# Kernel optimization log

Measured on AMD Instinct MI355X. Metric: run time of the kernel, lower is better.

The kernel has to match this reference:

```python
import jax, jax.numpy as jnp
import numpy as np

# static config (mirrors init_kwargs)
F_T, S = 8, 24            # video_shape = (F_T, S, S)
K, DIL = 3, 1             # kernel_size, dilation (same for all 3 axes)
HEADS, DHEAD, DIM = 8, 64, 512
INNER = HEADS * DHEAD
PAD = DIL * (K - 1)       # causal: pad 2 at the FRONT of each spatial axis
KJ = K ** 3               # 27 neighbors per query
N_VID = F_T * S * S       # 4608 video tokens


def causal_pad(t):
    # t: [B, D, F, S, S] -> pad front of f/h/w axes (torch F.pad (PAD*?,0) causal layout)
    return jnp.pad(t, ((0, 0), (0, 0), (PAD, 0), (PAD, 0), (PAD, 0)))


def unfold3d(t):
    # torch unfoldNd equivalent. t: [B, D, F+PAD, S+PAD, S+PAD]
    # returns [B, N_VID, KJ, D]; kernel offsets ordered (kf, kh, kw) w fastest,
    # matching torch unfold's channel-major / kernel-minor layout after the
    # rearrange 'b (d j) i -> b i j d'.
    sl = []
    for i in range(K):
        for j in range(K):
            for kk in range(K):
                sl.append(t[:, :, i * DIL:i * DIL + F_T,
                                  j * DIL:j * DIL + S,
                                  kk * DIL:kk * DIL + S])
    u = jnp.stack(sl, axis=2)                      # [B, D, KJ, F, S, S]
    B, D = t.shape[0], t.shape[1]
    u = u.reshape(B, D, KJ, N_VID)
    return jnp.transpose(u, (0, 3, 2, 1))          # [B, N_VID, KJ, D]


def make_mask():
    # True where the neighbor falls into zero padding (out-of-range / future under causal pad)
    ones = jnp.ones((1, 1, F_T, S, S), jnp.float32)
    u = unfold3d(causal_pad(ones))[0, :, :, 0]     # [N_VID, KJ]
    m = u == 0.0
    return jnp.pad(m, ((0, 0), (1, 0)), constant_values=False)  # bos col never masked


def stable_softmax(t, alpha=32.0 ** 2):
    t = t / alpha
    t = t - jax.lax.stop_gradient(jnp.max(t, axis=-1, keepdims=True))
    return jax.nn.softmax(t * alpha, axis=-1)


def setup_inputs() -> dict:
    key = jax.random.key(0)
    ks = jax.random.split(key, 9)
    return {
        "x": jax.random.normal(ks[0], (1, N_VID + 1, DIM), jnp.float32),
        "Wq": jax.random.normal(ks[1], (DIM, INNER), jnp.float32) * 0.02,
        "Wkv": jax.random.normal(ks[2], (DIM, 2 * INNER), jnp.float32) * 0.02,
        "W_th": jax.random.normal(ks[3], (HEADS, HEADS), jnp.float32) * 0.2,
        "Wout": jax.random.normal(ks[4], (INNER, DIM), jnp.float32) * 0.02,
        "bout": jax.random.normal(ks[5], (DIM,), jnp.float32) * 0.02,
        "ax1": jax.random.normal(ks[6], (K, HEADS), jnp.float32),
        "ax2": jax.random.normal(ks[7], (K, HEADS), jnp.float32),
        "ax3": jax.random.normal(ks[8], (K, HEADS), jnp.float32),
    }


def reference(x, Wq, Wkv, W_th, Wout, bout, ax1, ax2, ax3):
    b, n, _ = x.shape                       # b=1, n = 1 + N_VID (no extra padding)
    h, d = HEADS, DHEAD
    scale = d ** -0.5

    q = x @ Wq
    k, v = jnp.split(x @ Wkv, 2, axis=-1)

    def to_heads(t):  # 'b n (h d) -> (b h) n d'
        return t.reshape(b, n, h, d).transpose(0, 2, 1, 3).reshape(b * h, n, d)

    q, k, v = map(to_heads, (q, k, v))
    q = q[:, 1:] * scale                    # drop bos query
    k_bos, v_bos = k[:, :1], v[:, :1]       # [bh, 1, d]
    k, v = k[:, 1:], v[:, 1:]

    def to_vid(t):  # 'b (f h w) d -> b d f h w'
        return t.reshape(b * h, F_T, S, S, d).transpose(0, 4, 1, 2, 3)

    ku = unfold3d(causal_pad(to_vid(k)))    # [bh, N, KJ, d]
    vu = unfold3d(causal_pad(to_vid(v)))
    N = ku.shape[1]

    kb = jnp.broadcast_to(k_bos[:, :, None, :], (b * h, N, 1, d))
    vb = jnp.broadcast_to(v_bos[:, :, None, :], (b * h, N, 1, d))
    ku = jnp.concatenate([kb, ku], axis=2)  # [bh, N, KJ+1, d]
    vu = jnp.concatenate([vb, vu], axis=2)

    sim = jnp.einsum('bid,bijd->bij', q, ku)                 # [bh, N, KJ+1]

    # axial relative position bias over the 3x3x3 kernel, pad 0 for bos column
    rel = (ax1[:, None, None, :] + ax2[None, :, None, :] + ax3[None, None, :, :])
    rel = rel.reshape(KJ, h)                                 # [27, h]
    bias = jnp.pad(rel.T[:, None, :], ((0, 0), (0, 0), (1, 0)))  # [h, 1, KJ+1]

    sim = sim.reshape(b, h, N, KJ + 1) + bias[None]
    mask = make_mask()                                       # [N, KJ+1]
    sim = jnp.where(mask[None, None], -jnp.finfo(sim.dtype).max, sim)

    attn = stable_softmax(sim)                               # [b, h, N, KJ+1]
    attn = jnp.einsum('hg,bgij->bhij', W_th, attn)           # talking heads 1x1 conv

    out = jnp.einsum('bhij,bhijd->bhid', attn, vu.reshape(b, h, N, KJ + 1, d))
    out = jnp.concatenate([v_bos.reshape(b, h, 1, d), out], axis=2)  # re-attach bos value
    out = out.transpose(0, 2, 1, 3).reshape(b, n, h * d)     # '(b h) n d -> b n (h d)'
    return out @ Wout + bout
```

## Files before the change

kernel.cpp:

```cpp
#include <hip/hip_runtime.h>
#include <hip/hip_bf16.h>


constexpr int TFR   = 8;
constexpr int SDIM  = 24;
constexpr int NVID  = TFR * SDIM * SDIM;
constexpr int NTOK  = NVID + 1;
constexpr int NH    = 8;
constexpr int DM    = 512;
constexpr int NJ    = 28;

typedef __attribute__((ext_vector_type(8))) short bf16x8;
typedef __attribute__((ext_vector_type(8))) unsigned short ushort8;
typedef __attribute__((ext_vector_type(4))) float f32x4;

typedef const __attribute__((address_space(1))) unsigned int* gas_ptr;
typedef __attribute__((address_space(3))) unsigned int* las_ptr;

__device__ __forceinline__ float bf2f(unsigned short u) {
    return __uint_as_float((unsigned)u << 16);
}
__device__ __forceinline__ unsigned short f2bf(float f) {
    __hip_bfloat16 h = __float2bfloat16(f);
    return reinterpret_cast<unsigned short&>(h);
}

__global__ __launch_bounds__(256)
void prep_w(const float* __restrict__ Wq, const float* __restrict__ Wkv,
            const float* __restrict__ Wout,
            __hip_bfloat16* __restrict__ Wqkvt, __hip_bfloat16* __restrict__ Woutt)
{
    __shared__ float t[32][33];
    const int tid = threadIdx.x;
    int tb = blockIdx.x;
    const float* W; __hip_bfloat16* Wt; int Nd, tX, rowOff;
    if (tb < 256)      { W = Wq;   Wt = Wqkvt; Nd = 512;  tX = 16; rowOff = 0;   }
    else if (tb < 768) { tb -= 256; W = Wkv;  Wt = Wqkvt; Nd = 1024; tX = 32; rowOff = 512; }
    else               { tb -= 768; W = Wout; Wt = Woutt; Nd = 512;  tX = 16; rowOff = 0;   }
    const int n0 = (tb % tX) * 32, k0 = (tb / tX) * 32;
    const int r  = tid >> 3;
    const int c4 = (tid & 7) * 4;
    const float4 v = *(const float4*)(W + (size_t)(k0 + r) * Nd + n0 + c4);
    t[r][c4 + 0] = v.x; t[r][c4 + 1] = v.y; t[r][c4 + 2] = v.z; t[r][c4 + 3] = v.w;
    __syncthreads();
    #pragma unroll
    for (int j = 0; j < 4; ++j)
        Wt[(size_t)(rowOff + n0 + r) * 512 + k0 + c4 + j] = __float2bfloat16(t[c4 + j][r]);
}

__global__ __launch_bounds__(256)
void gemm_qkv(const float* __restrict__ A, const __hip_bfloat16* __restrict__ Bt,
              float* __restrict__ Cq, __hip_bfloat16* __restrict__ Ckv, int M)
{
    constexpr int BM = 128, BN = 128, BK = 64, PITCH = 72, K = 512;
    __shared__ short As[BM * PITCH];
    __shared__ __align__(16) short Bs[BN * BK];

    const int tid  = threadIdx.x;
    const int m0   = blockIdx.x * BM;
    const int n0   = blockIdx.y * BN;
    const int lane = tid & 63;
    const int wave = tid >> 6;
    const int wm   = (wave >> 1) * 64;
    const int wn   = (wave & 1) * 64;
    const int col  = lane & 15;
    const int quad = lane >> 4;

    f32x4 acc[4][4] = {};

    for (int k0 = 0; k0 < K; k0 += BK) {
        #pragma unroll
        for (int it = 0; it < 4; ++it) {
            const int idx = it * 256 + tid;
            const int r   = idx >> 3;
            const int u   = (idx & 7) ^ (r & 7);
            const __hip_bfloat16* gp = Bt + (size_t)(n0 + r) * K + k0 + u * 8;
            __builtin_amdgcn_global_load_lds(
                (gas_ptr)gp, (las_ptr)&Bs[(it * 256 + wave * 64) * 8], 16, 0, 0);
        }
        #pragma unroll
        for (int r = 0; r < 4; ++r) {
            const int m  = (tid >> 3) + r * 32;
            const int k8 = (tid & 7) * 8;
            const int gm = (m0 + m < M) ? (m0 + m) : (M - 1);
            const float4 f0 = *(const float4*)(A + (size_t)gm * K + k0 + k8);
            const float4 f1 = *(const float4*)(A + (size_t)gm * K + k0 + k8 + 4);
            unsigned short v[8] = { f2bf(f0.x), f2bf(f0.y), f2bf(f0.z), f2bf(f0.w),
                                    f2bf(f1.x), f2bf(f1.y), f2bf(f1.z), f2bf(f1.w) };
            *(ushort8*)(&As[m * PITCH + k8]) = *(const ushort8*)v;
        }
        __syncthreads();

        #pragma unroll
        for (int ks = 0; ks < 2; ++ks) {
            bf16x8 af[4], bfr[4];
            #pragma unroll
            for (int mt = 0; mt < 4; ++mt)
                af[mt] = *(const bf16x8*)(&As[(wm + mt * 16 + col) * PITCH + ks * 32 + quad * 8]);
            #pragma unroll
            for (int nt = 0; nt < 4; ++nt) {
                const int r = wn + nt * 16 + col;
                const int u = (ks * 4 + quad) ^ (r & 7);
                bfr[nt] = *(const bf16x8*)(&Bs[r * BK + u * 8]);
            }
            #pragma unroll
            for (int mt = 0; mt < 4; ++mt)
                #pragma unroll
                for (int nt = 0; nt < 4; ++nt)
                    acc[mt][nt] = __builtin_amdgcn_mfma_f32_16x16x32_bf16(
                        af[mt], bfr[nt], acc[mt][nt], 0, 0, 0);
        }
        __syncthreads();
    }

    const bool isQ = (n0 < 512);
    #pragma unroll
    for (int mt = 0; mt < 4; ++mt) {
        #pragma unroll
        for (int r = 0; r < 4; ++r) {
            const int row = m0 + wm + mt * 16 + quad * 4 + r;
            if (row >= M) continue;
            #pragma unroll
            for (int nt = 0; nt < 4; ++nt) {
                const int cg = n0 + wn + nt * 16 + col;
                const float v = acc[mt][nt][r];
                if (isQ) Cq[(size_t)row * 512 + cg] = v * 0.125f;
                else     Ckv[(size_t)row * 1024 + (cg - 512)] = __float2bfloat16(v);
            }
        }
    }
}

__global__ __launch_bounds__(256)
void gemm_out(const __hip_bfloat16* __restrict__ A, const __hip_bfloat16* __restrict__ Bt,
              float* __restrict__ C, int M, const float* __restrict__ bias)
{
    constexpr int BM = 64, BN = 64, BK = 64, K = 512;
    __shared__ __align__(16) short As[BM * BK];
    __shared__ __align__(16) short Bs[BN * BK];

    const int tid  = threadIdx.x;
    const int m0   = blockIdx.x * BM;
    const int n0   = blockIdx.y * BN;
    const int lane = tid & 63;
    const int wave = tid >> 6;
    const int wm   = (wave >> 1) * 32;
    const int wn   = (wave & 1) * 32;
    const int col  = lane & 15;
    const int quad = lane >> 4;

    f32x4 acc[2][2] = {};

    for (int k0 = 0; k0 < K; k0 += BK) {
        #pragma unroll
        for (int it = 0; it < 2; ++it) {
            const int idx = it * 256 + tid;
            const int r   = idx >> 3;
            const int u   = (idx & 7) ^ (r & 7);
            const __hip_bfloat16* gp = A + (size_t)(m0 + r) * K + k0 + u * 8;
            __builtin_amdgcn_global_load_lds(
                (gas_ptr)gp, (las_ptr)&As[(it * 256 + wave * 64) * 8], 16, 0, 0);
        }
        #pragma unroll
        for (int it = 0; it < 2; ++it) {
            const int idx = it * 256 + tid;
            const int r   = idx >> 3;
            const int u   = (idx & 7) ^ (r & 7);
            const __hip_bfloat16* gp = Bt + (size_t)(n0 + r) * K + k0 + u * 8;
            __builtin_amdgcn_global_load_lds(
                (gas_ptr)gp, (las_ptr)&Bs[(it * 256 + wave * 64) * 8], 16, 0, 0);
        }
        __syncthreads();

        #pragma unroll
        for (int ks = 0; ks < 2; ++ks) {
            bf16x8 af[2], bfr[2];
            #pragma unroll
            for (int mt = 0; mt < 2; ++mt) {
                const int r = wm + mt * 16 + col;
                const int u = (ks * 4 + quad) ^ (r & 7);
                af[mt] = *(const bf16x8*)(&As[r * BK + u * 8]);
            }
            #pragma unroll
            for (int nt = 0; nt < 2; ++nt) {
                const int r = wn + nt * 16 + col;
                const int u = (ks * 4 + quad) ^ (r & 7);
                bfr[nt] = *(const bf16x8*)(&Bs[r * BK + u * 8]);
            }
            #pragma unroll
            for (int mt = 0; mt < 2; ++mt)
                #pragma unroll
                for (int nt = 0; nt < 2; ++nt)
                    acc[mt][nt] = __builtin_amdgcn_mfma_f32_16x16x32_bf16(
                        af[mt], bfr[nt], acc[mt][nt], 0, 0, 0);
        }
        __syncthreads();
    }

    #pragma unroll
    for (int mt = 0; mt < 2; ++mt) {
        #pragma unroll
        for (int r = 0; r < 4; ++r) {
            const int row = m0 + wm + mt * 16 + quad * 4 + r;
            if (row >= M) continue;
            #pragma unroll
            for (int nt = 0; nt < 2; ++nt) {
                const int cg = n0 + wn + nt * 16 + col;
                C[(size_t)row * 512 + cg] = acc[mt][nt][r] + bias[cg];
            }
        }
    }
}

__global__ __launch_bounds__(256)
void attn_v2(const float* __restrict__ Q, const __hip_bfloat16* __restrict__ KVb,
             __hip_bfloat16* __restrict__ O,
             const float* __restrict__ W_th,
             const float* __restrict__ ax1, const float* __restrict__ ax2,
             const float* __restrict__ ax3)
{
    __shared__ float attn_s[4][NH * NJ];
    __shared__ float mixed_s[4][NH * NJ];

    const int tid  = threadIdx.x;
    const int wave = tid >> 6;
    const int lane = tid & 63;
    const int g    = lane >> 3;
    const int s    = lane & 7;
    const int i    = __builtin_amdgcn_readfirstlane(blockIdx.x * 4 + (tid >> 6));
    const int qrow = i + 1;

    const int t  = i / (SDIM * SDIM);
    const int rm = i % (SDIM * SDIM);
    const int y  = rm / SDIM;
    const int x  = rm % SDIM;

    float qf[8];
    {
        const float4 q0 = *(const float4*)(Q + (size_t)qrow * DM + lane * 8);
        const float4 q1 = *(const float4*)(Q + (size_t)qrow * DM + lane * 8 + 4);
        qf[0] = q0.x; qf[1] = q0.y; qf[2] = q0.z; qf[3] = q0.w;
        qf[4] = q1.x; qf[5] = q1.y; qf[6] = q1.z; qf[7] = q1.w;
    }
    float a1[3], a2[3], a3[3];
    #pragma unroll
    for (int d = 0; d < 3; ++d) {
        a1[d] = ax1[d * NH + g];
        a2[d] = ax2[d * NH + g];
        a3[d] = ax3[d * NH + g];
    }

    float sim[NJ];
    #pragma unroll
    for (int j = 0; j < NJ; ++j) {
        int row; bool valid; float bias;
        if (j == 0) { row = 0; valid = true; bias = 0.f; }
        else {
            const int jp = j - 1;
            const int di = jp / 9, dj = (jp / 3) % 3, dk = jp % 3;
            const int tt = t + di - 2, yy = y + dj - 2, xx = x + dk - 2;
            valid = (tt >= 0) && (yy >= 0) && (xx >= 0);
            row = 1 + tt * SDIM * SDIM + yy * SDIM + xx;
            bias = a1[di] + a2[dj] + a3[dk];
        }
        if (valid) {
            const ushort8 kv = *(const ushort8*)(KVb + (size_t)row * 1024 + lane * 8);
            float p = 0.f;
            #pragma unroll
            for (int e = 0; e < 8; ++e) p += bf2f(kv[e]) * qf[e];
            p += __shfl_xor(p, 1);
            p += __shfl_xor(p, 2);
            p += __shfl_xor(p, 4);
            sim[j] = p + bias;
        } else {
            sim[j] = -1e30f;
        }
    }

    float m = -1e30f;
    #pragma unroll
    for (int j = 0; j < NJ; ++j) m = fmaxf(m, sim[j]);
    float ssum = 0.f;
    #pragma unroll
    for (int j = 0; j < NJ; ++j) { sim[j] = __expf(sim[j] - m); ssum += sim[j]; }
    const float inv = 1.f / ssum;
    #pragma unroll
    for (int j = 0; j < NJ; ++j) sim[j] *= inv;

    if (s == 0) {
        #pragma unroll
        for (int u = 0; u < 7; ++u) {
            f32x4 v4 = { sim[4*u], sim[4*u+1], sim[4*u+2], sim[4*u+3] };
            *(f32x4*)(&attn_s[wave][g * NJ + 4 * u]) = v4;
        }
    }
    __syncthreads();

    if (tid < NH * NJ) {
        const int h = tid / NJ, j = tid % NJ;
        #pragma unroll
        for (int q = 0; q < 4; ++q) {
            float acc = 0.f;
            #pragma unroll
            for (int gg = 0; gg < NH; ++gg)
                acc += W_th[h * NH + gg] * attn_s[q][gg * NJ + j];
            mixed_s[q][h * NJ + j] = acc;
        }
    }
    __syncthreads();

    float acc8[8] = {};
    #pragma unroll
    for (int j = 0; j < NJ; ++j) {
        int row; bool valid;
        if (j == 0) { row = 0; valid = true; }
        else {
            const int jp = j - 1;
            const int di = jp / 9, dj = (jp / 3) % 3, dk = jp % 3;
            const int tt = t + di - 2, yy = y + dj - 2, xx = x + dk - 2;
            valid = (tt >= 0) && (yy >= 0) && (xx >= 0);
            row = 1 + tt * SDIM * SDIM + yy * SDIM + xx;
        }
        if (valid) {
            const ushort8 vv = *(const ushort8*)(KVb + (size_t)row * 1024 + 512 + lane * 8);
            const float w = mixed_s[wave][g * NJ + j];
            #pragma unroll
            for (int e = 0; e < 8; ++e) acc8[e] += w * bf2f(vv[e]);
        }
    }

    unsigned short o[8];
    #pragma unroll
    for (int e = 0; e < 8; ++e) o[e] = f2bf(acc8[e]);
    *(ushort8*)(O + (size_t)qrow * DM + lane * 8) = *(const ushort8*)o;

    if (i == 0) {
        const ushort8 vb = *(const ushort8*)(KVb + 512 + lane * 8);
        *(ushort8*)(O + lane * 8) = vb;
    }
}

extern "C" void kernel_launch(void* const* d_in, const int* in_sizes, int n_in,
                              void* d_out, int out_size, void* d_ws, size_t ws_size,
                              hipStream_t stream)
{
    const float* x    = (const float*)d_in[0];
    const float* Wq   = (const float*)d_in[1];
    const float* Wkv  = (const float*)d_in[2];
    const float* W_th = (const float*)d_in[3];
    const float* Wout = (const float*)d_in[4];
    const float* bout = (const float*)d_in[5];
    const float* ax1  = (const float*)d_in[6];
    const float* ax2  = (const float*)d_in[7];
    const float* ax3  = (const float*)d_in[8];
    float* out = (float*)d_out;

    char* p = (char*)d_ws;
    float* Qf = (float*)p;                       p += (size_t)NTOK * DM * 4;
    __hip_bfloat16* KVb   = (__hip_bfloat16*)p;  p += (size_t)NTOK * 2 * DM * 2;
    __hip_bfloat16* Ob    = (__hip_bfloat16*)p;  p += (size_t)NTOK * DM * 2;
    __hip_bfloat16* Wqkvt = (__hip_bfloat16*)p;  p += (size_t)3 * DM * DM * 2;
    __hip_bfloat16* Woutt = (__hip_bfloat16*)p;  p += (size_t)DM * DM * 2;

    const dim3 blk(256);
    const int mtiles128 = (NTOK + 127) / 128;
    const int mtiles64  = (NTOK + 63) / 64;

    prep_w<<<1024, blk, 0, stream>>>(Wq, Wkv, Wout, Wqkvt, Woutt);

    gemm_qkv<<<dim3(mtiles128, 12), blk, 0, stream>>>(x, Wqkvt, Qf, KVb, NTOK);

    attn_v2<<<dim3(NVID / 4), blk, 0, stream>>>(Qf, KVb, Ob, W_th, ax1, ax2, ax3);

    gemm_out<<<dim3(mtiles64, 8), blk, 0, stream>>>(Ob, Woutt, out, NTOK, bout);
}
```

Measured before the change: 134.0 us.

## Process two adjacent queries per wave sharing overlapping K/V neighbor loads

Each wave now handles two horizontally adjacent query tokens, iterating over a 3x3x4 neighborhood so the shared 3x3x2 overlap of K and V rows is loaded once and used for both queries. Blocks cover 8 queries and are remapped with a bid permutation (bid&7)*72 + (bid>>3) to spread work across XCDs/caches. The talking-heads mixing hoists W_th into registers. This cuts global gather traffic per query, at the cost of more registers (two sim arrays, two accumulators) and half as many blocks.

```diff
diff --git a/kernel.cpp b/kernel.cpp
--- a/kernel.cpp
+++ b/kernel.cpp
@@ -213,128 +213,188 @@
 }
 
 __global__ __launch_bounds__(256)
-void attn_v2(const float* __restrict__ Q, const __hip_bfloat16* __restrict__ KVb,
+void attn_v3(const float* __restrict__ Q, const __hip_bfloat16* __restrict__ KVb,
              __hip_bfloat16* __restrict__ O,
              const float* __restrict__ W_th,
              const float* __restrict__ ax1, const float* __restrict__ ax2,
              const float* __restrict__ ax3)
 {
-    __shared__ float attn_s[4][NH * NJ];
-    __shared__ float mixed_s[4][NH * NJ];
+    __shared__ float attn_s[8][NH * NJ];
+    __shared__ float mixed_s[8][NH * NJ];
 
     const int tid  = threadIdx.x;
     const int wave = tid >> 6;
     const int lane = tid & 63;
     const int g    = lane >> 3;
     const int s    = lane & 7;
-    const int i    = __builtin_amdgcn_readfirstlane(blockIdx.x * 4 + (tid >> 6));
-    const int qrow = i + 1;
-
-    const int t  = i / (SDIM * SDIM);
-    const int rm = i % (SDIM * SDIM);
+
+    const int bid  = blockIdx.x;
+    const int bidp = (bid & 7) * 72 + (bid >> 3);
+    const int pair = __builtin_amdgcn_readfirstlane(bidp * 4 + wave);
+    const int ia   = pair * 2;
+    const int qa_row = ia + 1, qb_row = ia + 2;
+
+    const int t  = ia / (SDIM * SDIM);
+    const int rm = ia % (SDIM * SDIM);
     const int y  = rm / SDIM;
     const int x  = rm % SDIM;
 
-    float qf[8];
+    float qa[8], qb[8];
     {
-        const float4 q0 = *(const float4*)(Q + (size_t)qrow * DM + lane * 8);
-        const float4 q1 = *(const float4*)(Q + (size_t)qrow * DM + lane * 8 + 4);
-        qf[0] = q0.x; qf[1] = q0.y; qf[2] = q0.z; qf[3] = q0.w;
-        qf[4] = q1.x; qf[5] = q1.y; qf[6] = q1.z; qf[7] = q1.w;
-    }
-    float a1[3], a2[3], a3[3];
+        const float4 a0 = *(const float4*)(Q + (size_t)qa_row * DM + lane * 8);
+        const float4 a1_ = *(const float4*)(Q + (size_t)qa_row * DM + lane * 8 + 4);
+        const float4 b0 = *(const float4*)(Q + (size_t)qb_row * DM + lane * 8);
+        const float4 b1 = *(const float4*)(Q + (size_t)qb_row * DM + lane * 8 + 4);
+        qa[0]=a0.x; qa[1]=a0.y; qa[2]=a0.z; qa[3]=a0.w;
+        qa[4]=a1_.x; qa[5]=a1_.y; qa[6]=a1_.z; qa[7]=a1_.w;
+        qb[0]=b0.x; qb[1]=b0.y; qb[2]=b0.z; qb[3]=b0.w;
+        qb[4]=b1.x; qb[5]=b1.y; qb[6]=b1.z; qb[7]=b1.w;
+    }
+    float bx1[3], bx2[3], bx3[3];
     #pragma unroll
     for (int d = 0; d < 3; ++d) {
-        a1[d] = ax1[d * NH + g];
-        a2[d] = ax2[d * NH + g];
-        a3[d] = ax3[d * NH + g];
-    }
-
-    float sim[NJ];
+        bx1[d] = ax1[d * NH + g];
+        bx2[d] = ax2[d * NH + g];
+        bx3[d] = ax3[d * NH + g];
+    }
+
+    float sim_a[NJ], sim_b[NJ];
+
+    {
+        const ushort8 kv = *(const ushort8*)(KVb + lane * 8);
+        float kf[8];
+        #pragma unroll
+        for (int e = 0; e < 8; ++e) kf[e] = bf2f(kv[e]);
+        float pa = 0.f, pb = 0.f;
+        #pragma unroll
+        for (int e = 0; e < 8; ++e) { pa += kf[e] * qa[e]; pb += kf[e] * qb[e]; }
+        pa += __shfl_xor(pa, 1); pa += __shfl_xor(pa, 2); pa += __shfl_xor(pa, 4);
+        pb += __shfl_xor(pb, 1); pb += __shfl_xor(pb, 2); pb += __shfl_xor(pb, 4);
+        sim_a[0] = pa; sim_b[0] = pb;
+    }
+    #pragma unroll
+    for (int di = 0; di < 3; ++di)
+    #pragma unroll
+    for (int dj = 0; dj < 3; ++dj)
+    #pragma unroll
+    for (int dkp = 0; dkp < 4; ++dkp) {
+        const int tt = t + di - 2, yy = y + dj - 2, xxp = x + dkp - 2;
+        const bool valid = (tt >= 0) && (yy >= 0) && (xxp >= 0);
+        float pa = 0.f, pb = 0.f;
+        if (valid) {
+            const int row = 1 + tt * SDIM * SDIM + yy * SDIM + xxp;
+            const ushort8 kv = *(const ushort8*)(KVb + (size_t)row * 1024 + lane * 8);
+            float kf[8];
+            #pragma unroll
+            for (int e = 0; e < 8; ++e) kf[e] = bf2f(kv[e]);
+            if (dkp < 3) {
+                #pragma unroll
+                for (int e = 0; e < 8; ++e) pa += kf[e] * qa[e];
+                pa += __shfl_xor(pa, 1); pa += __shfl_xor(pa, 2); pa += __shfl_xor(pa, 4);
+            }
+            if (dkp > 0) {
+                #pragma unroll
+                for (int e = 0; e < 8; ++e) pb += kf[e] * qb[e];
+                pb += __shfl_xor(pb, 1); pb += __shfl_xor(pb, 2); pb += __shfl_xor(pb, 4);
+            }
+        }
+        if (dkp < 3)
+            sim_a[1 + di * 9 + dj * 3 + dkp] =
+                valid ? (pa + bx1[di] + bx2[dj] + bx3[dkp]) : -1e30f;
+        if (dkp > 0)
+            sim_b[1 + di * 9 + dj * 3 + (dkp - 1)] =
+                valid ? (pb + bx1[di] + bx2[dj] + bx3[dkp - 1]) : -1e30f;
+    }
+
+    float ma = -1e30f, mb = -1e30f;
+    #pragma unroll
+    for (int j = 0; j < NJ; ++j) { ma = fmaxf(ma, sim_a[j]); mb = fmaxf(mb, sim_b[j]); }
+    float sa = 0.f, sb = 0.f;
     #pragma unroll
     for (int j = 0; j < NJ; ++j) {
-        int row; bool valid; float bias;
-        if (j == 0) { row = 0; valid = true; bias = 0.f; }
-        else {
-            const int jp = j - 1;
-            const int di = jp / 9, dj = (jp / 3) % 3, dk = jp % 3;
-            const int tt = t + di - 2, yy = y + dj - 2, xx = x + dk - 2;
-            valid = (tt >= 0) && (yy >= 0) && (xx >= 0);
-            row = 1 + tt * SDIM * SDIM + yy * SDIM + xx;
-            bias = a1[di] + a2[dj] + a3[dk];
-        }
-        if (valid) {
-            const ushort8 kv = *(const ushort8*)(KVb + (size_t)row * 1024 + lane * 8);
-            float p = 0.f;
-            #pragma unroll
-            for (int e = 0; e < 8; ++e) p += bf2f(kv[e]) * qf[e];
-            p += __shfl_xor(p, 1);
-            p += __shfl_xor(p, 2);
-            p += __shfl_xor(p, 4);
-            sim[j] = p + bias;
-        } else {
-            sim[j] = -1e30f;
-        }
-    }
-
-    float m = -1e30f;
-    #pragma unroll
-    for (int j = 0; j < NJ; ++j) m = fmaxf(m, sim[j]);
-    float ssum = 0.f;
-    #pragma unroll
-    for (int j = 0; j < NJ; ++j) { sim[j] = __expf(sim[j] - m); ssum += sim[j]; }
-    const float inv = 1.f / ssum;
-    #pragma unroll
-    for (int j = 0; j < NJ; ++j) sim[j] *= inv;
+        sim_a[j] = __expf(sim_a[j] - ma); sa += sim_a[j];
+        sim_b[j] = __expf(sim_b[j] - mb); sb += sim_b[j];
+    }
+    const float ra = 1.f / sa, rb = 1.f / sb;
+    #pragma unroll
+    for (int j = 0; j < NJ; ++j) { sim_a[j] *= ra; sim_b[j] *= rb; }
 
     if (s == 0) {
         #pragma unroll
         for (int u = 0; u < 7; ++u) {
-            f32x4 v4 = { sim[4*u], sim[4*u+1], sim[4*u+2], sim[4*u+3] };
-            *(f32x4*)(&attn_s[wave][g * NJ + 4 * u]) = v4;
+            f32x4 v4 = { sim_a[4*u], sim_a[4*u+1], sim_a[4*u+2], sim_a[4*u+3] };
+            *(f32x4*)(&attn_s[wave * 2][g * NJ + 4 * u]) = v4;
+        }
+    } else if (s == 1) {
+        #pragma unroll
+        for (int u = 0; u < 7; ++u) {
+            f32x4 v4 = { sim_b[4*u], sim_b[4*u+1], sim_b[4*u+2], sim_b[4*u+3] };
+            *(f32x4*)(&attn_s[wave * 2 + 1][g * NJ + 4 * u]) = v4;
         }
     }
     __syncthreads();
 
     if (tid < NH * NJ) {
         const int h = tid / NJ, j = tid % NJ;
-        #pragma unroll
-        for (int q = 0; q < 4; ++q) {
+        float w[NH];
+        #pragma unroll
+        for (int gg = 0; gg < NH; ++gg) w[gg] = W_th[h * NH + gg];
+        #pragma unroll
+        for (int qs = 0; qs < 8; ++qs) {
             float acc = 0.f;
             #pragma unroll
             for (int gg = 0; gg < NH; ++gg)
-                acc += W_th[h * NH + gg] * attn_s[q][gg * NJ + j];
-            mixed_s[q][h * NJ + j] = acc;
+                acc += w[gg] * attn_s[qs][gg * NJ + j];
+            mixed_s[qs][h * NJ + j] = acc;
         }
     }
     __syncthreads();
 
-    float acc8[8] = {};
-    #pragma unroll
-    for (int j = 0; j < NJ; ++j) {
-        int row; bool valid;
-        if (j == 0) { row = 0; valid = true; }
-        else {
-            const int jp = j - 1;
-            const int di = jp / 9, dj = (jp / 3) % 3, dk = jp % 3;
-            const int tt = t + di - 2, yy = y + dj - 2, xx = x + dk - 2;
-            valid = (tt >= 0) && (yy >= 0) && (xx >= 0);
-            row = 1 + tt * SDIM * SDIM + yy * SDIM + xx;
-        }
+    float oa[8] = {}, ob[8] = {};
+    {
+        const ushort8 vv = *(const ushort8*)(KVb + 512 + lane * 8);
+        const float wa = mixed_s[wave * 2][g * NJ];
+        const float wb = mixed_s[wave * 2 + 1][g * NJ];
+        #pragma unroll
+        for (int e = 0; e < 8; ++e) {
+            const float vf = bf2f(vv[e]);
+            oa[e] += wa * vf; ob[e] += wb * vf;
+        }
+    }
+    #pragma unroll
+    for (int di = 0; di < 3; ++di)
+    #pragma unroll
+    for (int dj = 0; dj < 3; ++dj)
+    #pragma unroll
+    for (int dkp = 0; dkp < 4; ++dkp) {
+        const int tt = t + di - 2, yy = y + dj - 2, xxp = x + dkp - 2;
+        const bool valid = (tt >= 0) && (yy >= 0) && (xxp >= 0);
         if (valid) {
+            const int row = 1 + tt * SDIM * SDIM + yy * SDIM + xxp;
             const ushort8 vv = *(const ushort8*)(KVb + (size_t)row * 1024 + 512 + lane * 8);
-            const float w = mixed_s[wave][g * NJ + j];
-            #pragma unroll
-            for (int e = 0; e < 8; ++e) acc8[e] += w * bf2f(vv[e]);
-        }
-    }
-
-    unsigned short o[8];
-    #pragma unroll
-    for (int e = 0; e < 8; ++e) o[e] = f2bf(acc8[e]);
-    *(ushort8*)(O + (size_t)qrow * DM + lane * 8) = *(const ushort8*)o;
-
-    if (i == 0) {
+            float vf[8];
+            #pragma unroll
+            for (int e = 0; e < 8; ++e) vf[e] = bf2f(vv[e]);
+            if (dkp < 3) {
+                const float wa = mixed_s[wave * 2][g * NJ + 1 + di * 9 + dj * 3 + dkp];
+                #pragma unroll
+                for (int e = 0; e < 8; ++e) oa[e] += wa * vf[e];
+            }
+            if (dkp > 0) {
+                const float wb = mixed_s[wave * 2 + 1][g * NJ + 1 + di * 9 + dj * 3 + (dkp - 1)];
+                #pragma unroll
+                for (int e = 0; e < 8; ++e) ob[e] += wb * vf[e];
+            }
+        }
+    }
+
+    unsigned short outa[8], outb[8];
+    #pragma unroll
+    for (int e = 0; e < 8; ++e) { outa[e] = f2bf(oa[e]); outb[e] = f2bf(ob[e]); }
+    *(ushort8*)(O + (size_t)qa_row * DM + lane * 8) = *(const ushort8*)outa;
+    *(ushort8*)(O + (size_t)qb_row * DM + lane * 8) = *(const ushort8*)outb;
+
+    if (ia == 0) {
         const ushort8 vb = *(const ushort8*)(KVb + 512 + lane * 8);
         *(ushort8*)(O + lane * 8) = vb;
     }
@@ -370,7 +430,7 @@
 
     gemm_qkv<<<dim3(mtiles128, 12), blk, 0, stream>>>(x, Wqkvt, Qf, KVb, NTOK);
 
-    attn_v2<<<dim3(NVID / 4), blk, 0, stream>>>(Qf, KVb, Ob, W_th, ax1, ax2, ax3);
+    attn_v3<<<dim3(NVID / 8), blk, 0, stream>>>(Qf, KVb, Ob, W_th, ax1, ax2, ax3);
 
     gemm_out<<<dim3(mtiles64, 8), blk, 0, stream>>>(Ob, Woutt, out, NTOK, bout);
 }
```

Result: slower. 141.8 us (+5.8%).
